# Performance work log

Measured on AMD Instinct MI355X. Metric: run time of the kernel, lower is better.

## Reference

```python
import jax, jax.numpy as jnp
import numpy as np

B, K, D = 2048, 100000, 50  # batch, memory-bank size (num users), USER_VEC_DIM

def setup_inputs() -> dict:
    key = jax.random.key(0)
    k1, k2 = jax.random.split(key)
    x = jax.random.normal(k1, (B, D), dtype=jnp.float32)   # batch of user vectors
    M = jax.random.normal(k2, (K, D), dtype=jnp.float32)   # user_memory_vec bank
    return {"x": x, "M": M}

def reference(x, M):
    # Batched form of the per-item Python loop in call():
    #   mu = M @ u ; gamma = softmax(mu, axis=0) ; u_ = sum_k gamma_k * M[k]
    scores = jnp.einsum('bd,kd->bk', x, M)           # [B, K]
    attn = jax.nn.softmax(scores, axis=-1)           # softmax over memory slots
    u_ = jnp.einsum('bk,kd->bd', attn, M)            # attention readout [B, D]
    return jnp.concatenate([x, u_], axis=-1)         # [B, 2D]
```

## Files before the change

### kernel.cpp

```cpp
#include <hip/hip_runtime.h>
#include <hip/hip_bf16.h>
#include <math.h>

#define B_SZ 2048
#define K_SZ 100000
#define D_SZ 50
#define BT   64
#define CK   64
#define STR  72
#define MTS  78
#define SHIFT 30.0f
#define LOG2E 1.4426950408889634f
#define SHIFT_L2 43.280851226668905f
#define PSTRIDE 52
#define NCH   1563
#define IMG_CH 9216
#define IMG_BYTES ((size_t)NCH * IMG_CH * 2)
#define NSEG  18

typedef short short8 __attribute__((ext_vector_type(8)));
typedef short short4v __attribute__((ext_vector_type(4)));
typedef float f32x4 __attribute__((ext_vector_type(4)));

#if __has_builtin(__builtin_amdgcn_mfma_f32_16x16x16bf16_1k)
#define HAVE_BF16_K16 1
#else
#define HAVE_BF16_K16 0
#endif

__device__ __forceinline__ unsigned short bf16_rne(float f) {
    union { float f; unsigned int u; } v; v.f = f;
    unsigned int r = (v.u + 0x7fffu + ((v.u >> 16) & 1u)) >> 16;
    return (unsigned short)r;
}
__device__ __forceinline__ float bf16_to_f(unsigned short h) {
    union { unsigned int u; float f; } v; v.u = ((unsigned int)h) << 16;
    return v.f;
}

__device__ __forceinline__ void load_lds16(const void* g, void* l) {
    __builtin_amdgcn_global_load_lds(
        (const __attribute__((address_space(1))) unsigned int*)g,
        (__attribute__((address_space(3))) unsigned int*)l, 16, 0, 0);
}

__global__ __launch_bounds__(256)
void precompute_m(const float* __restrict__ M, unsigned short* __restrict__ img) {
    __shared__ __align__(16) unsigned short Mt[64 * MTS];
    const int t = threadIdx.x;
    const int c0 = blockIdx.x;
    const int k0 = c0 * 64;
    for (int i = t; i < (64 * MTS) / 2; i += 256) ((unsigned int*)Mt)[i] = 0;
    __syncthreads();
    unsigned int* gh = (unsigned int*)(img + (size_t)c0 * IMG_CH);
    for (int i = t; i < 64 * 36; i += 256) {
        int r = i / 36, cd = i - r * 36, c = cd * 2;
        int kg = k0 + r;
        unsigned int val = 0;
        if (kg < K_SZ && c < D_SZ) {
            float2 v = *(const float2*)&M[(size_t)kg * D_SZ + c];
            val = ((unsigned int)bf16_rne(v.y) << 16) | bf16_rne(v.x);
            Mt[c * MTS + r]       = (unsigned short)(val & 0xffffu);
            Mt[(c + 1) * MTS + r] = (unsigned short)(val >> 16);
        }
        gh[i] = val;
    }
    __syncthreads();
    unsigned int* gt = (unsigned int*)(img + (size_t)c0 * IMG_CH + 64 * STR);
    for (int i = t; i < 64 * 36; i += 256) {
        int r = i / 36, c = i - r * 36;
        gt[i] = *(const unsigned int*)&Mt[r * MTS + c * 2];
    }
}

__global__ __launch_bounds__(512, 4)
void attend_fast(const float* __restrict__ x, const unsigned short* __restrict__ img,
                 float* __restrict__ part, int slice) {
    __shared__ __align__(16) unsigned short lds[2 * IMG_CH];
    __shared__ float lsc[4][64];

    const int t = threadIdx.x;
    const int w = t >> 6, lane = t & 63;
    const int quad = lane >> 4, lq = lane & 15;

    const int bid = blockIdx.x;
    const int rr = bid >> 3;
    const int split = (rr >> 5) * 8 + (bid & 7);
    const int xtile = rr & 31;
    const int b0 = xtile * BT;
    const int kbeg = split * slice;
    const int kend = min(kbeg + slice, K_SZ);

    const int nt0 = (w & 1) * 2;
    const int mblk = w >> 1;

    short8 xh[2][2], xl[2][2];
    for (int j = 0; j < 2; ++j) {
        int row = b0 + (nt0 + j) * 16 + lq;
        const float* xr = x + (size_t)row * D_SZ;
        for (int ki = 0; ki < 2; ++ki) {
            int d0 = ki * 32 + quad * 8;
            float v[8];
#pragma unroll
            for (int e = 0; e < 8; ++e) v[e] = 0.f;
            if (d0 + 8 <= D_SZ) {
#pragma unroll
                for (int e = 0; e < 4; ++e) {
                    float2 f2 = *(const float2*)&xr[d0 + 2 * e];
                    v[2 * e] = f2.x; v[2 * e + 1] = f2.y;
                }
            } else if (d0 < D_SZ) {
                float2 f2 = *(const float2*)&xr[d0];
                v[0] = f2.x; v[1] = f2.y;
            }
            short8 sh, sl;
#pragma unroll
            for (int e = 0; e < 8; ++e) {
                unsigned short h = bf16_rne(v[e]);
                sh[e] = (short)h;
                sl[e] = (short)bf16_rne(v[e] - bf16_to_f(h));
            }
            xh[j][ki] = sh; xl[j][ki] = sl;
        }
    }

    f32x4 Uacc[2][4] = {};
    float lac[2] = {0.f, 0.f};

    const int ci0 = kbeg >> 6;
    const int nch = (kend - kbeg + CK - 1) / CK;
    const int r0 = bid % nch;

    {
        const unsigned short* g = img + (size_t)(ci0 + r0) * IMG_CH;
        for (int seg = w; seg < NSEG; seg += 8)
            load_lds16((const unsigned int*)(g + seg * 512) + lane * 4, lds + seg * 512);
    }

    for (int i = 0; i < nch; ++i) {
        const int par = i & 1;
        unsigned short* cur = lds + par * IMG_CH;
        unsigned short* nxt = lds + (par ^ 1) * IMG_CH;

        __builtin_amdgcn_s_waitcnt(0);
        __syncthreads();

        if (i + 1 < nch) {
            int cc = r0 + i + 1; if (cc >= nch) cc -= nch;
            const unsigned short* g = img + (size_t)(ci0 + cc) * IMG_CH;
            for (int seg = w; seg < NSEG; seg += 8)
                load_lds16((const unsigned int*)(g + seg * 512) + lane * 4, nxt + seg * 512);
        }

        const unsigned short* Mhi = cur;
        const unsigned short* Mt  = cur + 64 * STR;

        f32x4 S[2] = {};
#pragma unroll
        for (int ki = 0; ki < 2; ++ki) {
            int aoff = (mblk * 16 + lq) * STR + ki * 32 + quad * 8;
            short8 ah = *(const short8*)&Mhi[aoff];
#pragma unroll
            for (int j = 0; j < 2; ++j) {
                S[j] = __builtin_amdgcn_mfma_f32_16x16x32_bf16(ah, xh[j][ki], S[j], 0, 0, 0);
                S[j] = __builtin_amdgcn_mfma_f32_16x16x32_bf16(ah, xl[j][ki], S[j], 0, 0, 0);
            }
        }

#if HAVE_BF16_K16
        short4v pa[2];
#pragma unroll
        for (int j = 0; j < 2; ++j) {
            float p0 = __builtin_amdgcn_exp2f(fmaf(S[j][0], LOG2E, -SHIFT_L2));
            float p1 = __builtin_amdgcn_exp2f(fmaf(S[j][1], LOG2E, -SHIFT_L2));
            float p2 = __builtin_amdgcn_exp2f(fmaf(S[j][2], LOG2E, -SHIFT_L2));
            float p3 = __builtin_amdgcn_exp2f(fmaf(S[j][3], LOG2E, -SHIFT_L2));
            lac[j] += (p0 + p1) + (p2 + p3);
            __hip_bfloat162 q01 = __float22bfloat162_rn(make_float2(p0, p1));
            __hip_bfloat162 q23 = __float22bfloat162_rn(make_float2(p2, p3));
            union { short4v s; unsigned int u[2]; } pk;
            __builtin_memcpy(&pk.u[0], &q01, 4);
            __builtin_memcpy(&pk.u[1], &q23, 4);
            pa[j] = pk.s;
        }

#pragma unroll
        for (int dt = 0; dt < 4; ++dt) {
            short4v bm = *(const short4v*)&Mt[(dt * 16 + lq) * STR + mblk * 16 + quad * 4];
#pragma unroll
            for (int j = 0; j < 2; ++j)
                Uacc[j][dt] = __builtin_amdgcn_mfma_f32_16x16x16bf16_1k(pa[j], bm, Uacc[j][dt], 0, 0, 0);
        }
#else
        short8 pa[2];
#pragma unroll
        for (int j = 0; j < 2; ++j) {
            float p0 = __builtin_amdgcn_exp2f(fmaf(S[j][0], LOG2E, -SHIFT_L2));
            float p1 = __builtin_amdgcn_exp2f(fmaf(S[j][1], LOG2E, -SHIFT_L2));
            float p2 = __builtin_amdgcn_exp2f(fmaf(S[j][2], LOG2E, -SHIFT_L2));
            float p3 = __builtin_amdgcn_exp2f(fmaf(S[j][3], LOG2E, -SHIFT_L2));
            lac[j] += (p0 + p1) + (p2 + p3);
            __hip_bfloat162 q01 = __float22bfloat162_rn(make_float2(p0, p1));
            __hip_bfloat162 q23 = __float22bfloat162_rn(make_float2(p2, p3));
            union { short8 s; unsigned int u[4]; } pk;
            __builtin_memcpy(&pk.u[0], &q01, 4);
            __builtin_memcpy(&pk.u[1], &q23, 4);
            pk.u[2] = 0; pk.u[3] = 0;
            pa[j] = pk.s;
        }
#pragma unroll
        for (int dt = 0; dt < 4; ++dt) {
            short4v b4 = *(const short4v*)&Mt[(dt * 16 + lq) * STR + mblk * 16 + quad * 4];
            short8 b8;
#pragma unroll
            for (int e = 0; e < 4; ++e) { b8[e] = b4[e]; b8[e + 4] = 0; }
#pragma unroll
            for (int j = 0; j < 2; ++j)
                Uacc[j][dt] = __builtin_amdgcn_mfma_f32_16x16x32_bf16(pa[j], b8, Uacc[j][dt], 0, 0, 0);
        }
#endif
    }

    for (int j = 0; j < 2; ++j) {
        float v = lac[j];
        v += __shfl_xor(v, 16);
        v += __shfl_xor(v, 32);
        if (quad == 0) lsc[mblk][(nt0 + j) * 16 + lq] = v;
    }

    float* Ured = (float*)lds;
#pragma unroll
    for (int rnd = 0; rnd < 4; ++rnd) {
        __syncthreads();
        if (mblk == rnd) {
#pragma unroll
            for (int j = 0; j < 2; ++j)
#pragma unroll
                for (int dt = 0; dt < 4; ++dt)
#pragma unroll
                    for (int r4 = 0; r4 < 4; ++r4) {
                        int row = (nt0 + j) * 16 + quad * 4 + r4;
                        int col = dt * 16 + lq;
                        if (rnd == 0) Ured[row * 66 + col] = Uacc[j][dt][r4];
                        else          Ured[row * 66 + col] += Uacc[j][dt][r4];
                    }
        }
    }
    __syncthreads();

    float* pp = part + ((size_t)split * B_SZ + b0) * PSTRIDE;
    for (int i = t; i < 64 * D_SZ; i += 512) {
        int row = i / D_SZ, d = i - row * D_SZ;
        pp[(size_t)row * PSTRIDE + d] = Ured[row * 66 + d];
    }
    if (t < 64) {
        float Ls = lsc[0][t] + lsc[1][t] + lsc[2][t] + lsc[3][t];
        pp[(size_t)t * PSTRIDE + D_SZ] = Ls;
    }
}

__global__ __launch_bounds__(512, 4)
void attend_partial_v2(const float* __restrict__ x, const float* __restrict__ M,
                       float* __restrict__ part, int slice) {
    __shared__ __align__(16) unsigned short lds[4 * 64 * STR];
    __shared__ float lsc[4][64];
    unsigned short* bufA  = lds;
    unsigned short* bufB  = lds + 64 * STR;
    unsigned short* Mc_hi = lds + 2 * 64 * STR;
    unsigned short* Mc_lo = lds + 3 * 64 * STR;

    const int t = threadIdx.x;
    const int w = t >> 6, lane = t & 63;
    const int quad = lane >> 4, lq = lane & 15;
    const int b0 = blockIdx.x * 64;
    const int split = blockIdx.y;
    const int kbeg = split * slice;
    const int kend = min(kbeg + slice, K_SZ);

    for (int i = t; i < 4 * 64 * STR; i += 512) lds[i] = 0;
    __syncthreads();
    for (int i = t; i < 64 * 25; i += 512) {
        int r = i / 25, cp = i - r * 25, c = cp * 2;
        float2 v = *(const float2*)&x[(size_t)(b0 + r) * D_SZ + c];
        unsigned short h0 = bf16_rne(v.x), h1 = bf16_rne(v.y);
        unsigned short l0 = bf16_rne(v.x - bf16_to_f(h0));
        unsigned short l1 = bf16_rne(v.y - bf16_to_f(h1));
        *(unsigned int*)&bufA[r * STR + c] = ((unsigned int)h1 << 16) | h0;
        *(unsigned int*)&bufB[r * STR + c] = ((unsigned int)l1 << 16) | l0;
    }
    __syncthreads();

    const int nt0 = (w & 1) * 2;
    const int mblk = w >> 1;
    short8 xh[2][2], xl[2][2];
    for (int j = 0; j < 2; ++j)
        for (int ki = 0; ki < 2; ++ki) {
            int off = ((nt0 + j) * 16 + lq) * STR + ki * 32 + quad * 8;
            xh[j][ki] = *(const short8*)&bufA[off];
            xl[j][ki] = *(const short8*)&bufB[off];
        }

    f32x4 Uacc[2] = {};
    float lac[2] = {0.f, 0.f};

    for (int k0 = kbeg; k0 < kend; k0 += CK) {
        __syncthreads();
        for (int i = t; i < 64 * 25; i += 512) {
            int r = i / 25, cp = i - r * 25, c = cp * 2;
            int kg = k0 + r;
            float2 v = make_float2(0.f, 0.f);
            if (kg < kend) v = *(const float2*)&M[(size_t)kg * D_SZ + c];
            unsigned short h0 = bf16_rne(v.x), h1 = bf16_rne(v.y);
            unsigned short l0 = bf16_rne(v.x - bf16_to_f(h0));
            unsigned short l1 = bf16_rne(v.y - bf16_to_f(h1));
            *(unsigned int*)&Mc_hi[r * STR + c] = ((unsigned int)h1 << 16) | h0;
            *(unsigned int*)&Mc_lo[r * STR + c] = ((unsigned int)l1 << 16) | l0;
            bufB[c * STR + r] = h0;
            bufB[(c + 1) * STR + r] = h1;
        }
        __syncthreads();

        f32x4 S[2] = {};
        for (int ki = 0; ki < 2; ++ki) {
            int aoff = (mblk * 16 + lq) * STR + ki * 32 + quad * 8;
            short8 ah = *(const short8*)&Mc_hi[aoff];
            short8 al = *(const short8*)&Mc_lo[aoff];
            for (int j = 0; j < 2; ++j) {
                S[j] = __builtin_amdgcn_mfma_f32_16x16x32_bf16(ah, xh[j][ki], S[j], 0, 0, 0);
                S[j] = __builtin_amdgcn_mfma_f32_16x16x32_bf16(ah, xl[j][ki], S[j], 0, 0, 0);
                S[j] = __builtin_amdgcn_mfma_f32_16x16x32_bf16(al, xh[j][ki], S[j], 0, 0, 0);
            }
        }
        for (int j = 0; j < 2; ++j) {
            unsigned short pb4[4];
#pragma unroll
            for (int r4 = 0; r4 < 4; ++r4) {
                float p = __expf(S[j][r4] - SHIFT);
                lac[j] += p;
                pb4[r4] = bf16_rne(p);
            }
            int b = (nt0 + j) * 16 + lq;
            int n0 = mblk * 16 + quad * 4;
            *(unsigned int*)&bufA[b * STR + n0]     = ((unsigned int)pb4[1] << 16) | pb4[0];
            *(unsigned int*)&bufA[b * STR + n0 + 2] = ((unsigned int)pb4[3] << 16) | pb4[2];
        }
        __syncthreads();
        for (int ki = 0; ki < 2; ++ki) {
            int poff = (mblk * 16 + lq) * STR + ki * 32 + quad * 8;
            short8 ap = *(const short8*)&bufA[poff];
            for (int j = 0; j < 2; ++j) {
                int doff = ((nt0 + j) * 16 + lq) * STR + ki * 32 + quad * 8;
                short8 bm = *(const short8*)&bufB[doff];
                Uacc[j] = __builtin_amdgcn_mfma_f32_16x16x32_bf16(ap, bm, Uacc[j], 0, 0, 0);
            }
        }
    }

    for (int j = 0; j < 2; ++j) {
        float v = lac[j];
        v += __shfl_xor(v, 16);
        v += __shfl_xor(v, 32);
        if (quad == 0) lsc[mblk][(nt0 + j) * 16 + lq] = v;
    }
    __syncthreads();
    float* pp = part + ((size_t)split * B_SZ + b0) * PSTRIDE;
    for (int j = 0; j < 2; ++j) {
        int d = (nt0 + j) * 16 + lq;
        if (d < D_SZ) {
#pragma unroll
            for (int r4 = 0; r4 < 4; ++r4) {
                int b = mblk * 16 + quad * 4 + r4;
                pp[(size_t)b * PSTRIDE + d] = Uacc[j][r4];
            }
        }
    }
    if (t < 64) {
        float Ls = lsc[0][t] + lsc[1][t] + lsc[2][t] + lsc[3][t];
        pp[(size_t)t * PSTRIDE + D_SZ] = Ls;
    }
}

__global__ __launch_bounds__(256)
void combine(const float* __restrict__ x, const float* __restrict__ part,
             float* __restrict__ out, int nsplit) {
    const int b = blockIdx.x * 4 + (threadIdx.x >> 6);
    const int t = threadIdx.x & 63;
    float L = 0.f;
    for (int s = 0; s < nsplit; ++s)
        L += part[((size_t)s * B_SZ + b) * PSTRIDE + D_SZ];
    if (t < D_SZ) {
        float acc = 0.f;
        for (int s = 0; s < nsplit; ++s)
            acc += part[((size_t)s * B_SZ + b) * PSTRIDE + t];
        out[(size_t)b * (2 * D_SZ) + t] = x[(size_t)b * D_SZ + t];
        out[(size_t)b * (2 * D_SZ) + D_SZ + t] = acc / L;
    }
}

extern "C" void kernel_launch(void* const* d_in, const int* in_sizes, int n_in,
                              void* d_out, int out_size, void* d_ws, size_t ws_size,
                              hipStream_t stream) {
    const float* x = (const float*)d_in[0];
    const float* M = (const float*)d_in[1];
    float* out = (float*)d_out;
    const size_t per_split = (size_t)B_SZ * PSTRIDE * sizeof(float);

    if (ws_size >= IMG_BYTES + 8 * per_split) {
        unsigned short* img = (unsigned short*)d_ws;
        float* part = (float*)((char*)d_ws + IMG_BYTES);
        int ns = (int)((ws_size - IMG_BYTES) / per_split);
        if (ns > 32) ns = 32;
        ns &= ~7;
        int slice = (((K_SZ + ns - 1) / ns) + 63) & ~63;
        precompute_m<<<NCH, 256, 0, stream>>>(M, img);
        attend_fast<<<32 * ns, 512, 0, stream>>>(x, img, part, slice);
        combine<<<B_SZ / 4, 256, 0, stream>>>(x, part, out, ns);
    } else {
        float* part = (float*)d_ws;
        int ns = (int)(ws_size / per_split);
        if (ns > 32) ns = 32;
        if (ns < 1) ns = 1;
        int slice = (K_SZ + ns - 1) / ns;
        dim3 gridA(B_SZ / 64, ns);
        attend_partial_v2<<<gridA, 512, 0, stream>>>(x, M, part, slice);
        combine<<<B_SZ / 4, 256, 0, stream>>>(x, part, out, ns);
    }
}
```

Measured before the change: 193.3 us.

## Halve batch tile in attend_fast to double grid size and occupancy

Shrinks the batch tile per block from 64 to 32 rows, so each wave handles one 16-row tile instead of two. The grid doubles and launch bounds ask for 8 blocks per CU, aiming for more parallelism and fewer registers per wave. In exchange, every M chunk is streamed from global into LDS twice as often, which doubles memory traffic and halves the reuse per loaded chunk. BT is still used by other kernels through the shared macro, so the fallback path may be affected.

```diff
diff --git a/kernel.cpp b/kernel.cpp
--- a/kernel.cpp
+++ b/kernel.cpp
@@ -5,7 +5,7 @@
 #define B_SZ 2048
 #define K_SZ 100000
 #define D_SZ 50
-#define BT   64
+#define BT   32
 #define CK   64
 #define STR  72
 #define MTS  78
@@ -73,11 +73,11 @@
     }
 }
 
-__global__ __launch_bounds__(512, 4)
+__global__ __launch_bounds__(512, 8)
 void attend_fast(const float* __restrict__ x, const unsigned short* __restrict__ img,
                  float* __restrict__ part, int slice) {
     __shared__ __align__(16) unsigned short lds[2 * IMG_CH];
-    __shared__ float lsc[4][64];
+    __shared__ float lsc[4][BT];
 
     const int t = threadIdx.x;
     const int w = t >> 6, lane = t & 63;
@@ -85,18 +85,18 @@
 
     const int bid = blockIdx.x;
     const int rr = bid >> 3;
-    const int split = (rr >> 5) * 8 + (bid & 7);
-    const int xtile = rr & 31;
+    const int split = (rr >> 6) * 8 + (bid & 7);
+    const int xtile = rr & 63;
     const int b0 = xtile * BT;
     const int kbeg = split * slice;
     const int kend = min(kbeg + slice, K_SZ);
 
-    const int nt0 = (w & 1) * 2;
+    const int jt = w & 1;
     const int mblk = w >> 1;
 
-    short8 xh[2][2], xl[2][2];
-    for (int j = 0; j < 2; ++j) {
-        int row = b0 + (nt0 + j) * 16 + lq;
+    short8 xh[2], xl[2];
+    {
+        int row = b0 + jt * 16 + lq;
         const float* xr = x + (size_t)row * D_SZ;
         for (int ki = 0; ki < 2; ++ki) {
             int d0 = ki * 32 + quad * 8;
@@ -120,12 +120,12 @@
                 sh[e] = (short)h;
                 sl[e] = (short)bf16_rne(v[e] - bf16_to_f(h));
             }
-            xh[j][ki] = sh; xl[j][ki] = sl;
-        }
-    }
-
-    f32x4 Uacc[2][4] = {};
-    float lac[2] = {0.f, 0.f};
+            xh[ki] = sh; xl[ki] = sl;
+        }
+    }
+
+    f32x4 Uacc[4] = {};
+    float lac = 0.f;
 
     const int ci0 = kbeg >> 6;
     const int nch = (kend - kbeg + CK - 1) / CK;
@@ -155,58 +155,51 @@
         const unsigned short* Mhi = cur;
         const unsigned short* Mt  = cur + 64 * STR;
 
-        f32x4 S[2] = {};
+        f32x4 S = {};
 #pragma unroll
         for (int ki = 0; ki < 2; ++ki) {
             int aoff = (mblk * 16 + lq) * STR + ki * 32 + quad * 8;
             short8 ah = *(const short8*)&Mhi[aoff];
-#pragma unroll
-            for (int j = 0; j < 2; ++j) {
-                S[j] = __builtin_amdgcn_mfma_f32_16x16x32_bf16(ah, xh[j][ki], S[j], 0, 0, 0);
-                S[j] = __builtin_amdgcn_mfma_f32_16x16x32_bf16(ah, xl[j][ki], S[j], 0, 0, 0);
-            }
+            S = __builtin_amdgcn_mfma_f32_16x16x32_bf16(ah, xh[ki], S, 0, 0, 0);
+            S = __builtin_amdgcn_mfma_f32_16x16x32_bf16(ah, xl[ki], S, 0, 0, 0);
         }
 
 #if HAVE_BF16_K16
-        short4v pa[2];
-#pragma unroll
-        for (int j = 0; j < 2; ++j) {
-            float p0 = __builtin_amdgcn_exp2f(fmaf(S[j][0], LOG2E, -SHIFT_L2));
-            float p1 = __builtin_amdgcn_exp2f(fmaf(S[j][1], LOG2E, -SHIFT_L2));
-            float p2 = __builtin_amdgcn_exp2f(fmaf(S[j][2], LOG2E, -SHIFT_L2));
-            float p3 = __builtin_amdgcn_exp2f(fmaf(S[j][3], LOG2E, -SHIFT_L2));
-            lac[j] += (p0 + p1) + (p2 + p3);
+        short4v pa;
+        {
+            float p0 = __builtin_amdgcn_exp2f(fmaf(S[0], LOG2E, -SHIFT_L2));
+            float p1 = __builtin_amdgcn_exp2f(fmaf(S[1], LOG2E, -SHIFT_L2));
+            float p2 = __builtin_amdgcn_exp2f(fmaf(S[2], LOG2E, -SHIFT_L2));
+            float p3 = __builtin_amdgcn_exp2f(fmaf(S[3], LOG2E, -SHIFT_L2));
+            lac += (p0 + p1) + (p2 + p3);
             __hip_bfloat162 q01 = __float22bfloat162_rn(make_float2(p0, p1));
             __hip_bfloat162 q23 = __float22bfloat162_rn(make_float2(p2, p3));
             union { short4v s; unsigned int u[2]; } pk;
             __builtin_memcpy(&pk.u[0], &q01, 4);
             __builtin_memcpy(&pk.u[1], &q23, 4);
-            pa[j] = pk.s;
+            pa = pk.s;
         }
 
 #pragma unroll
         for (int dt = 0; dt < 4; ++dt) {
             short4v bm = *(const short4v*)&Mt[(dt * 16 + lq) * STR + mblk * 16 + quad * 4];
-#pragma unroll
-            for (int j = 0; j < 2; ++j)
-                Uacc[j][dt] = __builtin_amdgcn_mfma_f32_16x16x16bf16_1k(pa[j], bm, Uacc[j][dt], 0, 0, 0);
+            Uacc[dt] = __builtin_amdgcn_mfma_f32_16x16x16bf16_1k(pa, bm, Uacc[dt], 0, 0, 0);
         }
 #else
-        short8 pa[2];
-#pragma unroll
-        for (int j = 0; j < 2; ++j) {
-            float p0 = __builtin_amdgcn_exp2f(fmaf(S[j][0], LOG2E, -SHIFT_L2));
-            float p1 = __builtin_amdgcn_exp2f(fmaf(S[j][1], LOG2E, -SHIFT_L2));
-            float p2 = __builtin_amdgcn_exp2f(fmaf(S[j][2], LOG2E, -SHIFT_L2));
-            float p3 = __builtin_amdgcn_exp2f(fmaf(S[j][3], LOG2E, -SHIFT_L2));
-            lac[j] += (p0 + p1) + (p2 + p3);
+        short8 pa;
+        {
+            float p0 = __builtin_amdgcn_exp2f(fmaf(S[0], LOG2E, -SHIFT_L2));
+            float p1 = __builtin_amdgcn_exp2f(fmaf(S[1], LOG2E, -SHIFT_L2));
+            float p2 = __builtin_amdgcn_exp2f(fmaf(S[2], LOG2E, -SHIFT_L2));
+            float p3 = __builtin_amdgcn_exp2f(fmaf(S[3], LOG2E, -SHIFT_L2));
+            lac += (p0 + p1) + (p2 + p3);
             __hip_bfloat162 q01 = __float22bfloat162_rn(make_float2(p0, p1));
             __hip_bfloat162 q23 = __float22bfloat162_rn(make_float2(p2, p3));
             union { short8 s; unsigned int u[4]; } pk;
             __builtin_memcpy(&pk.u[0], &q01, 4);
             __builtin_memcpy(&pk.u[1], &q23, 4);
             pk.u[2] = 0; pk.u[3] = 0;
-            pa[j] = pk.s;
+            pa = pk.s;
         }
 #pragma unroll
         for (int dt = 0; dt < 4; ++dt) {
@@ -214,18 +207,16 @@
             short8 b8;
 #pragma unroll
             for (int e = 0; e < 4; ++e) { b8[e] = b4[e]; b8[e + 4] = 0; }
-#pragma unroll
-            for (int j = 0; j < 2; ++j)
-                Uacc[j][dt] = __builtin_amdgcn_mfma_f32_16x16x32_bf16(pa[j], b8, Uacc[j][dt], 0, 0, 0);
+            Uacc[dt] = __builtin_amdgcn_mfma_f32_16x16x32_bf16(pa, b8, Uacc[dt], 0, 0, 0);
         }
 #endif
     }
 
-    for (int j = 0; j < 2; ++j) {
-        float v = lac[j];
+    {
+        float v = lac;
         v += __shfl_xor(v, 16);
         v += __shfl_xor(v, 32);
-        if (quad == 0) lsc[mblk][(nt0 + j) * 16 + lq] = v;
+        if (quad == 0) lsc[mblk][jt * 16 + lq] = v;
     }
 
     float* Ured = (float*)lds;
@@ -234,26 +225,24 @@
         __syncthreads();
         if (mblk == rnd) {
 #pragma unroll
-            for (int j = 0; j < 2; ++j)
-#pragma unroll
-                for (int dt = 0; dt < 4; ++dt)
-#pragma unroll
-                    for (int r4 = 0; r4 < 4; ++r4) {
-                        int row = (nt0 + j) * 16 + quad * 4 + r4;
-                        int col = dt * 16 + lq;
-                        if (rnd == 0) Ured[row * 66 + col] = Uacc[j][dt][r4];
-                        else          Ured[row * 66 + col] += Uacc[j][dt][r4];
-                    }
+            for (int dt = 0; dt < 4; ++dt)
+#pragma unroll
+                for (int r4 = 0; r4 < 4; ++r4) {
+                    int row = jt * 16 + quad * 4 + r4;
+                    int col = dt * 16 + lq;
+                    if (rnd == 0) Ured[row * 66 + col] = Uacc[dt][r4];
+                    else          Ured[row * 66 + col] += Uacc[dt][r4];
+                }
         }
     }
     __syncthreads();
 
     float* pp = part + ((size_t)split * B_SZ + b0) * PSTRIDE;
-    for (int i = t; i < 64 * D_SZ; i += 512) {
+    for (int i = t; i < BT * D_SZ; i += 512) {
         int row = i / D_SZ, d = i - row * D_SZ;
         pp[(size_t)row * PSTRIDE + d] = Ured[row * 66 + d];
     }
-    if (t < 64) {
+    if (t < BT) {
         float Ls = lsc[0][t] + lsc[1][t] + lsc[2][t] + lsc[3][t];
         pp[(size_t)t * PSTRIDE + D_SZ] = Ls;
     }
@@ -413,7 +402,7 @@
         ns &= ~7;
         int slice = (((K_SZ + ns - 1) / ns) + 63) & ~63;
         precompute_m<<<NCH, 256, 0, stream>>>(M, img);
-        attend_fast<<<32 * ns, 512, 0, stream>>>(x, img, part, slice);
+        attend_fast<<<64 * ns, 512, 0, stream>>>(x, img, part, slice);
         combine<<<B_SZ / 4, 256, 0, stream>>>(x, part, out, ns);
     } else {
         float* part = (float*)d_ws;
```

Result: slower. 208.9 us (+8.0%).

## Double memory chunk to 128 keys and use full K32 MFMA for readout

Applied to the files above, without the earlier changes.

The fast path now processes 128 memory rows per pipeline step instead of 64. The precomputed bf16 image is repacked into 128-row chunks, with the transposed part stored at a wider stride. The softmax weights for two 16-row sub-tiles are shuffled across lanes with ds_bpermute to form full 32-wide operands, so the readout uses 16x16x32 MFMAs instead of 16x16x16 or zero-padded ones. This halves the per-chunk barriers and loop iterations and removes wasted MFMA work, at the cost of a larger LDS footprint and extra permute instructions.

```diff
diff --git a/kernel.cpp b/kernel.cpp
--- a/kernel.cpp
+++ b/kernel.cpp
@@ -6,27 +6,23 @@
 #define K_SZ 100000
 #define D_SZ 50
 #define BT   64
-#define CK   64
+#define CK   128
 #define STR  72
+#define MTSTR 136
 #define MTS  78
 #define SHIFT 30.0f
 #define LOG2E 1.4426950408889634f
 #define SHIFT_L2 43.280851226668905f
 #define PSTRIDE 52
-#define NCH   1563
-#define IMG_CH 9216
-#define IMG_BYTES ((size_t)NCH * IMG_CH * 2)
-#define NSEG  18
+#define NCH2  782
+#define NCHH  1564
+#define IMG_CH 17920
+#define IMG_BYTES ((size_t)NCH2 * IMG_CH * 2)
+#define NSEG  35
 
 typedef short short8 __attribute__((ext_vector_type(8)));
 typedef short short4v __attribute__((ext_vector_type(4)));
 typedef float f32x4 __attribute__((ext_vector_type(4)));
-
-#if __has_builtin(__builtin_amdgcn_mfma_f32_16x16x16bf16_1k)
-#define HAVE_BF16_K16 1
-#else
-#define HAVE_BF16_K16 0
-#endif
 
 __device__ __forceinline__ unsigned short bf16_rne(float f) {
     union { float f; unsigned int u; } v; v.f = f;
@@ -49,10 +45,11 @@
     __shared__ __align__(16) unsigned short Mt[64 * MTS];
     const int t = threadIdx.x;
     const int c0 = blockIdx.x;
+    const int ci = c0 >> 1, h = c0 & 1;
     const int k0 = c0 * 64;
     for (int i = t; i < (64 * MTS) / 2; i += 256) ((unsigned int*)Mt)[i] = 0;
     __syncthreads();
-    unsigned int* gh = (unsigned int*)(img + (size_t)c0 * IMG_CH);
+    unsigned int* gh = (unsigned int*)(img + (size_t)ci * IMG_CH + h * (64 * STR));
     for (int i = t; i < 64 * 36; i += 256) {
         int r = i / 36, cd = i - r * 36, c = cd * 2;
         int kg = k0 + r;
@@ -66,10 +63,10 @@
         gh[i] = val;
     }
     __syncthreads();
-    unsigned int* gt = (unsigned int*)(img + (size_t)c0 * IMG_CH + 64 * STR);
-    for (int i = t; i < 64 * 36; i += 256) {
-        int r = i / 36, c = i - r * 36;
-        gt[i] = *(const unsigned int*)&Mt[r * MTS + c * 2];
+    unsigned int* gt = (unsigned int*)(img + (size_t)ci * IMG_CH + 128 * STR);
+    for (int i = t; i < 64 * 32; i += 256) {
+        int r = i >> 5, c = i & 31;
+        gt[(size_t)r * (MTSTR / 2) + h * 32 + c] = *(const unsigned int*)&Mt[r * MTS + c * 2];
     }
 }
 
@@ -127,7 +124,7 @@
     f32x4 Uacc[2][4] = {};
     float lac[2] = {0.f, 0.f};
 
-    const int ci0 = kbeg >> 6;
+    const int ci0 = kbeg >> 7;
     const int nch = (kend - kbeg + CK - 1) / CK;
     const int r0 = bid % nch;
 
@@ -153,72 +150,68 @@
         }
 
         const unsigned short* Mhi = cur;
-        const unsigned short* Mt  = cur + 64 * STR;
-
-        f32x4 S[2] = {};
-#pragma unroll
-        for (int ki = 0; ki < 2; ++ki) {
-            int aoff = (mblk * 16 + lq) * STR + ki * 32 + quad * 8;
-            short8 ah = *(const short8*)&Mhi[aoff];
+        const unsigned short* Mt  = cur + 128 * STR;
+
+        f32x4 S[2][2] = {};
+#pragma unroll
+        for (int s = 0; s < 2; ++s)
+#pragma unroll
+            for (int ki = 0; ki < 2; ++ki) {
+                int aoff = (mblk * 32 + s * 16 + lq) * STR + ki * 32 + quad * 8;
+                short8 ah = *(const short8*)&Mhi[aoff];
+#pragma unroll
+                for (int j = 0; j < 2; ++j) {
+                    S[s][j] = __builtin_amdgcn_mfma_f32_16x16x32_bf16(ah, xh[j][ki], S[s][j], 0, 0, 0);
+                    S[s][j] = __builtin_amdgcn_mfma_f32_16x16x32_bf16(ah, xl[j][ki], S[s][j], 0, 0, 0);
+                }
+            }
+
+        int PA[2][2], PB[2][2];
+#pragma unroll
+        for (int s = 0; s < 2; ++s)
 #pragma unroll
             for (int j = 0; j < 2; ++j) {
-                S[j] = __builtin_amdgcn_mfma_f32_16x16x32_bf16(ah, xh[j][ki], S[j], 0, 0, 0);
-                S[j] = __builtin_amdgcn_mfma_f32_16x16x32_bf16(ah, xl[j][ki], S[j], 0, 0, 0);
-            }
-        }
-
-#if HAVE_BF16_K16
-        short4v pa[2];
+                float p0 = __builtin_amdgcn_exp2f(fmaf(S[s][j][0], LOG2E, -SHIFT_L2));
+                float p1 = __builtin_amdgcn_exp2f(fmaf(S[s][j][1], LOG2E, -SHIFT_L2));
+                float p2 = __builtin_amdgcn_exp2f(fmaf(S[s][j][2], LOG2E, -SHIFT_L2));
+                float p3 = __builtin_amdgcn_exp2f(fmaf(S[s][j][3], LOG2E, -SHIFT_L2));
+                lac[j] += (p0 + p1) + (p2 + p3);
+                __hip_bfloat162 q01 = __float22bfloat162_rn(make_float2(p0, p1));
+                __hip_bfloat162 q23 = __float22bfloat162_rn(make_float2(p2, p3));
+                int u01, u23;
+                __builtin_memcpy(&u01, &q01, 4);
+                __builtin_memcpy(&u23, &q23, 4);
+                PA[s][j] = u01; PB[s][j] = u23;
+            }
+
+        const int o1 = (((quad & 1) << 5) + lq) << 2;
+        const int shi = quad >> 1;
+        short8 pa[2];
 #pragma unroll
         for (int j = 0; j < 2; ++j) {
-            float p0 = __builtin_amdgcn_exp2f(fmaf(S[j][0], LOG2E, -SHIFT_L2));
-            float p1 = __builtin_amdgcn_exp2f(fmaf(S[j][1], LOG2E, -SHIFT_L2));
-            float p2 = __builtin_amdgcn_exp2f(fmaf(S[j][2], LOG2E, -SHIFT_L2));
-            float p3 = __builtin_amdgcn_exp2f(fmaf(S[j][3], LOG2E, -SHIFT_L2));
-            lac[j] += (p0 + p1) + (p2 + p3);
-            __hip_bfloat162 q01 = __float22bfloat162_rn(make_float2(p0, p1));
-            __hip_bfloat162 q23 = __float22bfloat162_rn(make_float2(p2, p3));
-            union { short4v s; unsigned int u[2]; } pk;
-            __builtin_memcpy(&pk.u[0], &q01, 4);
-            __builtin_memcpy(&pk.u[1], &q23, 4);
-            pa[j] = pk.s;
+            int a0 = __builtin_amdgcn_ds_bpermute(o1,      PA[0][j]);
+            int a1 = __builtin_amdgcn_ds_bpermute(o1,      PA[1][j]);
+            int b0 = __builtin_amdgcn_ds_bpermute(o1,      PB[0][j]);
+            int b1 = __builtin_amdgcn_ds_bpermute(o1,      PB[1][j]);
+            int c0 = __builtin_amdgcn_ds_bpermute(o1 + 64, PA[0][j]);
+            int c1 = __builtin_amdgcn_ds_bpermute(o1 + 64, PA[1][j]);
+            int d0 = __builtin_amdgcn_ds_bpermute(o1 + 64, PB[0][j]);
+            int d1 = __builtin_amdgcn_ds_bpermute(o1 + 64, PB[1][j]);
+            union { short8 s8; int u[4]; } pk;
+            pk.u[0] = shi ? a1 : a0;
+            pk.u[1] = shi ? b1 : b0;
+            pk.u[2] = shi ? c1 : c0;
+            pk.u[3] = shi ? d1 : d0;
+            pa[j] = pk.s8;
         }
 
 #pragma unroll
         for (int dt = 0; dt < 4; ++dt) {
-            short4v bm = *(const short4v*)&Mt[(dt * 16 + lq) * STR + mblk * 16 + quad * 4];
+            short8 bm = *(const short8*)&Mt[(dt * 16 + lq) * MTSTR + mblk * 32 + quad * 8];
 #pragma unroll
             for (int j = 0; j < 2; ++j)
-                Uacc[j][dt] = __builtin_amdgcn_mfma_f32_16x16x16bf16_1k(pa[j], bm, Uacc[j][dt], 0, 0, 0);
-        }
-#else
-        short8 pa[2];
-#pragma unroll
-        for (int j = 0; j < 2; ++j) {
-            float p0 = __builtin_amdgcn_exp2f(fmaf(S[j][0], LOG2E, -SHIFT_L2));
-            float p1 = __builtin_amdgcn_exp2f(fmaf(S[j][1], LOG2E, -SHIFT_L2));
-            float p2 = __builtin_amdgcn_exp2f(fmaf(S[j][2], LOG2E, -SHIFT_L2));
-            float p3 = __builtin_amdgcn_exp2f(fmaf(S[j][3], LOG2E, -SHIFT_L2));
-            lac[j] += (p0 + p1) + (p2 + p3);
-            __hip_bfloat162 q01 = __float22bfloat162_rn(make_float2(p0, p1));
-            __hip_bfloat162 q23 = __float22bfloat162_rn(make_float2(p2, p3));
-            union { short8 s; unsigned int u[4]; } pk;
-            __builtin_memcpy(&pk.u[0], &q01, 4);
-            __builtin_memcpy(&pk.u[1], &q23, 4);
-            pk.u[2] = 0; pk.u[3] = 0;
-            pa[j] = pk.s;
-        }
-#pragma unroll
-        for (int dt = 0; dt < 4; ++dt) {
-            short4v b4 = *(const short4v*)&Mt[(dt * 16 + lq) * STR + mblk * 16 + quad * 4];
-            short8 b8;
-#pragma unroll
-            for (int e = 0; e < 4; ++e) { b8[e] = b4[e]; b8[e + 4] = 0; }
-#pragma unroll
-            for (int j = 0; j < 2; ++j)
-                Uacc[j][dt] = __builtin_amdgcn_mfma_f32_16x16x32_bf16(pa[j], b8, Uacc[j][dt], 0, 0, 0);
-        }
-#endif
+                Uacc[j][dt] = __builtin_amdgcn_mfma_f32_16x16x32_bf16(pa[j], bm, Uacc[j][dt], 0, 0, 0);
+        }
     }
 
     for (int j = 0; j < 2; ++j) {
@@ -249,11 +242,11 @@
     __syncthreads();
 
     float* pp = part + ((size_t)split * B_SZ + b0) * PSTRIDE;
-    for (int i = t; i < 64 * D_SZ; i += 512) {
+    for (int i = t; i < BT * D_SZ; i += 512) {
         int row = i / D_SZ, d = i - row * D_SZ;
         pp[(size_t)row * PSTRIDE + d] = Ured[row * 66 + d];
     }
-    if (t < 64) {
+    if (t < BT) {
         float Ls = lsc[0][t] + lsc[1][t] + lsc[2][t] + lsc[3][t];
         pp[(size_t)t * PSTRIDE + D_SZ] = Ls;
     }
@@ -303,7 +296,7 @@
     f32x4 Uacc[2] = {};
     float lac[2] = {0.f, 0.f};
 
-    for (int k0 = kbeg; k0 < kend; k0 += CK) {
+    for (int k0 = kbeg; k0 < kend; k0 += 64) {
         __syncthreads();
         for (int i = t; i < 64 * 25; i += 512) {
             int r = i / 25, cp = i - r * 25, c = cp * 2;
@@ -411,8 +404,8 @@
         int ns = (int)((ws_size - IMG_BYTES) / per_split);
         if (ns > 32) ns = 32;
         ns &= ~7;
-        int slice = (((K_SZ + ns - 1) / ns) + 63) & ~63;
-        precompute_m<<<NCH, 256, 0, stream>>>(M, img);
+        int slice = (((K_SZ + ns - 1) / ns) + 127) & ~127;
+        precompute_m<<<NCHH, 256, 0, stream>>>(M, img);
         attend_fast<<<32 * ns, 512, 0, stream>>>(x, img, part, slice);
         combine<<<B_SZ / 4, 256, 0, stream>>>(x, part, out, ns);
     } else {
```

After: 204.2 us. 5.6% more time.

## Accumulate split partials with atomics and fix split count at 32

Applied to the files above, without the earlier changes.

The fast attention kernel now atomically adds its per-split partial numerators and softmax denominators into a single zeroed buffer, instead of writing one slice per split. The combine kernel therefore reads one row per batch element instead of looping over all splits. The split count is hard-coded to 32 and launch bounds are raised to request 8 blocks per CU. This costs an extra memset and many float atomics per block, makes the summation order nondeterministic, and the higher occupancy hint may force register spills.

```diff
diff --git a/kernel.cpp b/kernel.cpp
--- a/kernel.cpp
+++ b/kernel.cpp
@@ -17,6 +17,7 @@
 #define IMG_CH 9216
 #define IMG_BYTES ((size_t)NCH * IMG_CH * 2)
 #define NSEG  18
+#define PART_BYTES ((size_t)B_SZ * PSTRIDE * sizeof(float))
 
 typedef short short8 __attribute__((ext_vector_type(8)));
 typedef short short4v __attribute__((ext_vector_type(4)));
@@ -73,7 +74,7 @@
     }
 }
 
-__global__ __launch_bounds__(512, 4)
+__global__ __launch_bounds__(512, 8)
 void attend_fast(const float* __restrict__ x, const unsigned short* __restrict__ img,
                  float* __restrict__ part, int slice) {
     __shared__ __align__(16) unsigned short lds[2 * IMG_CH];
@@ -248,14 +249,14 @@
     }
     __syncthreads();
 
-    float* pp = part + ((size_t)split * B_SZ + b0) * PSTRIDE;
-    for (int i = t; i < 64 * D_SZ; i += 512) {
+    float* pp = part + (size_t)b0 * PSTRIDE;
+    for (int i = t; i < BT * D_SZ; i += 512) {
         int row = i / D_SZ, d = i - row * D_SZ;
-        pp[(size_t)row * PSTRIDE + d] = Ured[row * 66 + d];
-    }
-    if (t < 64) {
+        atomicAdd(&pp[(size_t)row * PSTRIDE + d], Ured[row * 66 + d]);
+    }
+    if (t < BT) {
         float Ls = lsc[0][t] + lsc[1][t] + lsc[2][t] + lsc[3][t];
-        pp[(size_t)t * PSTRIDE + D_SZ] = Ls;
+        atomicAdd(&pp[(size_t)t * PSTRIDE + D_SZ], Ls);
     }
 }
 
@@ -381,6 +382,19 @@
 }
 
 __global__ __launch_bounds__(256)
+void combine_norm(const float* __restrict__ x, const float* __restrict__ part,
+                  float* __restrict__ out) {
+    const int b = blockIdx.x * 4 + (threadIdx.x >> 6);
+    const int t = threadIdx.x & 63;
+    if (t < D_SZ) {
+        float L = part[(size_t)b * PSTRIDE + D_SZ];
+        float acc = part[(size_t)b * PSTRIDE + t];
+        out[(size_t)b * (2 * D_SZ) + t] = x[(size_t)b * D_SZ + t];
+        out[(size_t)b * (2 * D_SZ) + D_SZ + t] = acc / L;
+    }
+}
+
+__global__ __launch_bounds__(256)
 void combine(const float* __restrict__ x, const float* __restrict__ part,
              float* __restrict__ out, int nsplit) {
     const int b = blockIdx.x * 4 + (threadIdx.x >> 6);
@@ -405,16 +419,15 @@
     float* out = (float*)d_out;
     const size_t per_split = (size_t)B_SZ * PSTRIDE * sizeof(float);
 
-    if (ws_size >= IMG_BYTES + 8 * per_split) {
+    if (ws_size >= IMG_BYTES + PART_BYTES) {
         unsigned short* img = (unsigned short*)d_ws;
         float* part = (float*)((char*)d_ws + IMG_BYTES);
-        int ns = (int)((ws_size - IMG_BYTES) / per_split);
-        if (ns > 32) ns = 32;
-        ns &= ~7;
+        const int ns = 32;
         int slice = (((K_SZ + ns - 1) / ns) + 63) & ~63;
         precompute_m<<<NCH, 256, 0, stream>>>(M, img);
+        hipMemsetAsync(part, 0, PART_BYTES, stream);
         attend_fast<<<32 * ns, 512, 0, stream>>>(x, img, part, slice);
-        combine<<<B_SZ / 4, 256, 0, stream>>>(x, part, out, ns);
+        combine_norm<<<B_SZ / 4, 256, 0, stream>>>(x, part, out);
     } else {
         float* part = (float*)d_ws;
         int ns = (int)(ws_size / per_split);
```

After: 633.6 us. 3.28x slower.
